# Optimization experiments

Measured on AMD Instinct MI355X. Metric: run time of the kernel, lower is better.

## Reference

```python
import jax, jax.numpy as jnp
import numpy as np

CONF = 0.3      # confidence threshold (NMS.conf)
IOU = 0.6       # IoU threshold (NMS.iou)
MAX_WH = 4096.0 # class-offset trick for per-class NMS
K = 2048        # max candidates entering NMS (yolov5-style cap)
MAX_DET = 300   # max detections kept per image (fixed output size)


def setup_inputs() -> dict:
    key = jax.random.key(0)
    kxy, kwh, kobj, kcls = jax.random.split(key, 4)
    B, N, NC = 8, 25200, 80
    # realistic raw predictions: xywh in pixel units for a 640x640 image
    xy = jax.random.uniform(kxy, (B, N, 2), minval=0.0, maxval=640.0)
    wh = jax.random.uniform(kwh, (B, N, 2), minval=2.0, maxval=160.0)
    obj = jax.random.uniform(kobj, (B, N, 1))
    cls = jax.random.uniform(kcls, (B, N, NC))
    x = jnp.concatenate([xy, wh, obj, cls], axis=-1)  # [B, N, 5+NC]
    return {"x": x}


def _xywh2xyxy(b):
    xy, half = b[..., :2], b[..., 2:4] * 0.5
    return jnp.concatenate([xy - half, xy + half], axis=-1)


def _pairwise_iou(boxes):  # boxes: [K, 4] xyxy -> [K, K]
    lt = jnp.maximum(boxes[:, None, :2], boxes[None, :, :2])
    rb = jnp.minimum(boxes[:, None, 2:], boxes[None, :, 2:])
    inter = jnp.clip(rb - lt, 0.0).prod(-1)
    area = (boxes[:, 2] - boxes[:, 0]) * (boxes[:, 3] - boxes[:, 1])
    return inter / (area[:, None] + area[None, :] - inter + 1e-9)


def _nms_single(pred):  # pred: [N, 5+NC]
    obj = pred[:, 4]
    cls_conf = pred[:, 5:] * obj[:, None]          # conf = obj * cls prob
    conf = cls_conf.max(-1)
    cls_id = jnp.argmax(cls_conf, -1)
    valid = (obj > CONF) & (conf > CONF)           # candidate + final threshold
    boxes = _xywh2xyxy(pred[:, :4])
    scores = jnp.where(valid, conf, -1.0)
    top_s, idx = jax.lax.top_k(scores, K)          # cap candidates, sorted desc
    boxes_k = boxes[idx]
    cls_k = cls_id[idx]
    valid_k = top_s > 0.0
    # offset boxes by class so NMS is per-class
    shifted = boxes_k + cls_k[:, None].astype(boxes_k.dtype) * MAX_WH
    iou = _pairwise_iou(shifted)                   # [K, K]
    order = jnp.arange(K)

    def body(keep, i):  # greedy suppression in score order
        active = keep[i] & valid_k[i]
        sup = (iou[i] > IOU) & (order > i)
        keep = jnp.where(active, keep & ~sup, keep)
        return keep, None

    keep, _ = jax.lax.scan(body, jnp.ones((K,), bool), order)
    keep = keep & valid_k
    final_s = jnp.where(keep, top_s, -1.0)
    det_s, det_i = jax.lax.top_k(final_s, MAX_DET)
    dets = jnp.concatenate(
        [boxes_k[det_i], top_s[det_i][:, None],
         cls_k[det_i][:, None].astype(boxes_k.dtype)], axis=-1)  # [MAX_DET, 6]
    return dets, det_s > 0.0


def reference(x):
    # returns (dets [B, MAX_DET, 6] = xyxy,conf,cls ; valid mask [B, MAX_DET])
    return jax.vmap(_nms_single)(x)
```

## Files before the change

kernel.cpp:

```cpp
#include <hip/hip_runtime.h>

#define B 8
#define N 25200
#define ROW 85
#define NC 80
#define K 2048
#define MAXDET 300
#define NBUCKET 16384
#define CAND_CAP 4096
#define NCHUNK 32
#define STILE 64
#define CTR_STRIDE 64

__global__ void __launch_bounds__(256)
nms_score_kernel(const float* __restrict__ x,
                 float* __restrict__ scores,
                 int* __restrict__ cls_id,
                 float4* __restrict__ boxes4,
                 unsigned* __restrict__ ready,
                 unsigned* __restrict__ done_ctr) {
    int b = blockIdx.y;
    int i0 = blockIdx.x * STILE;
    if (blockIdx.x == 0 && threadIdx.x == 0) {
        ready[b * CTR_STRIDE] = 0u;
        done_ctr[b * CTR_STRIDE] = 0u;
    }
    int rows = N - i0; if (rows > STILE) rows = STILE;
    __shared__ float lx[STILE * ROW];
    {
        const float4* s4 = (const float4*)(x + ((size_t)b * N + i0) * ROW);
        float4* d4 = (float4*)lx;
        int nv = rows * ROW / 4;
        for (int k = threadIdx.x; k < nv; k += 256) d4[k] = s4[k];
    }
    __syncthreads();
    int g = threadIdx.x >> 2;
    int q = threadIdx.x & 3;
    if (g >= rows) return;
    const float* p = lx + g * ROW;
    float obj = p[4];
    float best = -1e30f;
    int bc = 127;
    if (obj > 0.3f) {
        #pragma unroll
        for (int k = 0; k < 20; ++k) {
            int c = q + 4 * k;
            float v = __fmul_rn(p[5 + c], obj);
            if (v > best) { best = v; bc = c; }
        }
    }
    #pragma unroll
    for (int m = 1; m < 4; m <<= 1) {
        float ov = __shfl_xor(best, m, 64);
        int   oc = __shfl_xor(bc, m, 64);
        if (ov > best || (ov == best && oc < bc)) { best = ov; bc = oc; }
    }
    if (q == 0) {
        int i = i0 + g;
        float score = (obj > 0.3f && best > 0.3f) ? best : -1.0f;
        scores[b * N + i] = score;
        cls_id[b * N + i] = (bc == 127) ? 0 : bc;
        float cx = p[0], cy = p[1], w = p[2], h = p[3];
        float hx = __fmul_rn(w, 0.5f);
        float hy = __fmul_rn(h, 0.5f);
        boxes4[b * N + i] = make_float4(__fsub_rn(cx, hx), __fsub_rn(cy, hy),
                                        __fadd_rn(cx, hx), __fadd_rn(cy, hy));
    }
}

__global__ void __launch_bounds__(1024, 1)
nms_tail_kernel(const float* __restrict__ scores,
                const float4* __restrict__ boxes4,
                const int* __restrict__ cls_id,
                unsigned long long* __restrict__ gkeys,
                unsigned long long* __restrict__ keepbits,
                unsigned* __restrict__ ready,
                unsigned* __restrict__ done_ctr,
                float* __restrict__ out) {
    __shared__ union {
        struct {
            unsigned loff[NBUCKET];
            unsigned lcnt16[NBUCKET / 2];
            unsigned long long lk[CAND_CAP];
        } s;
        struct {
            unsigned long long keys[K];
            unsigned long long lcm[NC * NCHUNK];
        } c;
    } U;
    __shared__ unsigned wsum[16];

    int bid = blockIdx.x;
    int t = threadIdx.x;
    int ln = t & 63, wv = t >> 6;
    unsigned long long below = (ln == 0) ? 0ULL : (~0ULL >> (64 - ln));

    if (bid < B) {
        int b = bid;
        constexpr int NITER = (N + 1023) / 1024;

        if (t < NCHUNK) keepbits[b * NCHUNK + t] = 0ULL;
        {
            uint4 z = {0u, 0u, 0u, 0u};
            uint4* d1 = (uint4*)U.s.loff;
            for (int k = t; k < (NBUCKET + NBUCKET / 2) / 4; k += 1024) d1[k] = z;
        }
        for (int k = t; k < CAND_CAP; k += 1024) U.s.lk[k] = 0ULL;
        __syncthreads();

        float sreg[NITER];
        #pragma unroll
        for (int r = 0; r < NITER; ++r) {
            int i = t + r * 1024;
            float s = (i < N) ? scores[b * N + i] : -1.0f;
            sreg[r] = s;
            if (s > 0.0f) {
                int q = (int)(__fmul_rn(s, 16384.0f));
                if (q > NBUCKET - 1) q = NBUCKET - 1;
                atomicAdd(&U.s.loff[q], 1u);
            }
        }
        __syncthreads();

        unsigned v[16];
        unsigned A4 = (unsigned)(NBUCKET - 16 - t * 16) / 4;
        {
            uint4 u0 = ((uint4*)U.s.loff)[A4 + 0];
            uint4 u1 = ((uint4*)U.s.loff)[A4 + 1];
            uint4 u2 = ((uint4*)U.s.loff)[A4 + 2];
            uint4 u3 = ((uint4*)U.s.loff)[A4 + 3];
            unsigned u[16] = {u0.x,u0.y,u0.z,u0.w, u1.x,u1.y,u1.z,u1.w,
                              u2.x,u2.y,u2.z,u2.w, u3.x,u3.y,u3.z,u3.w};
            #pragma unroll
            for (int k = 0; k < 16; ++k) v[k] = u[15 - k];
        }
        unsigned S = 0;
        #pragma unroll
        for (int k = 0; k < 16; ++k) S += v[k];
        unsigned pref = S;
        #pragma unroll
        for (int o = 1; o < 64; o <<= 1) { unsigned u = __shfl_up(pref, o, 64); if (ln >= o) pref += u; }
        if (ln == 63) wsum[wv] = pref;
        __syncthreads();
        unsigned wbase = 0;
        for (int w = 0; w < wv; ++w) wbase += wsum[w];
        unsigned running = wbase + pref - S;
        {
            unsigned o[16];
            #pragma unroll
            for (int k = 0; k < 16; ++k) { o[15 - k] = running; running += v[k]; }
            ((uint4*)U.s.loff)[A4 + 0] = make_uint4(o[0],  o[1],  o[2],  o[3]);
            ((uint4*)U.s.loff)[A4 + 1] = make_uint4(o[4],  o[5],  o[6],  o[7]);
            ((uint4*)U.s.loff)[A4 + 2] = make_uint4(o[8],  o[9],  o[10], o[11]);
            ((uint4*)U.s.loff)[A4 + 3] = make_uint4(o[12], o[13], o[14], o[15]);
        }
        __syncthreads();

        #pragma unroll
        for (int r = 0; r < NITER; ++r) {
            float s = sreg[r];
            if (s > 0.0f) {
                int i = t + r * 1024;
                int q = (int)(__fmul_rn(s, 16384.0f));
                if (q > NBUCKET - 1) q = NBUCKET - 1;
                unsigned start = U.s.loff[q];
                if (start < CAND_CAP) {
                    unsigned sh = (q & 1) * 16;
                    unsigned old = atomicAdd(&U.s.lcnt16[q >> 1], 1u << sh);
                    unsigned rank = (old >> sh) & 0xFFFFu;
                    unsigned pos = start + rank;
                    if (pos < CAND_CAP) {
                        unsigned long long key =
                            ((unsigned long long)__float_as_uint(s) << 32) | (unsigned)(~i);
                        U.s.lk[pos] = key;
                    }
                }
            }
        }
        __syncthreads();

        for (int q = t; q < NBUCKET; q += 1024) {
            unsigned start = U.s.loff[q];
            if (start < CAND_CAP) {
                unsigned c = (U.s.lcnt16[q >> 1] >> ((q & 1) * 16)) & 0xFFFFu;
                unsigned m = c;
                if (m > CAND_CAP - start) m = CAND_CAP - start;
                if (m >= 2) {
                    for (unsigned a = start + 1; a < start + m; ++a) {
                        unsigned long long kv = U.s.lk[a];
                        unsigned p2 = a;
                        while (p2 > start && U.s.lk[p2 - 1] < kv) { U.s.lk[p2] = U.s.lk[p2 - 1]; --p2; }
                        U.s.lk[p2] = kv;
                    }
                }
            }
        }
        __syncthreads();

        for (int r = t; r < K; r += 1024)
            gkeys[(size_t)b * K + r] = U.s.lk[r];
        __syncthreads();
        if (t == 0) {
            __threadfence();
            atomicExch(&ready[b * CTR_STRIDE], 1u);
        }
        return;
    }

    int gid = bid - B;
    int b = gid / 5;
    int grp = gid % 5;
    int c = grp * 16 + wv;

    if (t == 0) {
        while (atomicOr(&ready[b * CTR_STRIDE], 0u) == 0u)
            __builtin_amdgcn_s_sleep(8);
        __threadfence();
    }
    __syncthreads();

    for (int r = t; r < K; r += 1024) U.c.keys[r] = gkeys[(size_t)b * K + r];
    for (int k = t; k < NC * NCHUNK; k += 1024) U.c.lcm[k] = 0ULL;
    __syncthreads();

    for (int r = t; r < K; r += 1024) {
        unsigned long long key = U.c.keys[r];
        if (key != 0ULL) {
            int idx = (int)(~(unsigned)key);
            int cc = cls_id[b * N + idx];
            atomicOr(&U.c.lcm[cc * NCHUNK + (r >> 6)], 1ULL << (r & 63));
        }
    }
    __syncthreads();

    int n = 0, r = -1, ch_i = -1, myk = -1;
    unsigned long long mych = 0ULL;
    for (int ch = 0; ch < NCHUNK; ++ch) {
        unsigned long long m = U.c.lcm[c * NCHUNK + ch];
        int cnt = __popcll(m);
        if (myk < 0 && ln < n + cnt) { mych = m; myk = ln - n; ch_i = ch; }
        n += cnt;
    }
    if (myk >= 0) {
        unsigned long long mm = mych;
        for (int z = 0; z < myk; ++z) mm &= mm - 1;
        r = ch_i * 64 + (int)__builtin_ctzll(mm);
    }

    float shf = __fmul_rn((float)c, 4096.0f);

    if (n > 0 && n <= 64) {
        float x1 = 0.f, y1 = 0.f, x2 = 0.f, y2 = 0.f, ar = 0.f;
        if (ln < n) {
            unsigned long long key = U.c.keys[r];
            int idx = (int)(~(unsigned)key);
            float4 bb = boxes4[(size_t)b * N + idx];
            x1 = __fadd_rn(bb.x, shf); y1 = __fadd_rn(bb.y, shf);
            x2 = __fadd_rn(bb.z, shf); y2 = __fadd_rn(bb.w, shf);
            ar = __fmul_rn(__fsub_rn(x2, x1), __fsub_rn(y2, y1));
        }
        unsigned long long keepw = (n == 64) ? ~0ULL : ((1ULL << n) - 1ULL);
        for (int i = 0; i < n; ++i) {
            if (!((keepw >> i) & 1ULL)) continue;
            float bx1 = __shfl(x1, i, 64), by1 = __shfl(y1, i, 64);
            float bx2 = __shfl(x2, i, 64), by2 = __shfl(y2, i, 64);
            float ba  = __shfl(ar, i, 64);
            bool cond = false;
            if (ln > i && ln < n) {
                float lx = fmaxf(bx1, x1), ly = fmaxf(by1, y1);
                float rx = fminf(bx2, x2), ry = fminf(by2, y2);
                float w = fmaxf(__fsub_rn(rx, lx), 0.0f);
                float h = fmaxf(__fsub_rn(ry, ly), 0.0f);
                float inter = __fmul_rn(w, h);
                float denom = __fadd_rn(__fsub_rn(__fadd_rn(ba, ar), inter), 1e-9f);
                cond = __fdiv_rn(inter, denom) > 0.6f;
            }
            keepw &= ~__ballot(cond);
        }
        if (ln < n && ((keepw >> ln) & 1ULL))
            atomicOr(&keepbits[b * NCHUNK + (r >> 6)], 1ULL << (r & 63));
    } else if (n > 64) {
        unsigned long long membw = (ln < NCHUNK) ? U.c.lcm[c * NCHUNK + ln] : 0ULL;
        unsigned long long keepw2 = membw;
        for (int i = 0; i < K; ++i) {
            int ch = i >> 6;
            unsigned long long mw = __shfl(membw, ch, 64);
            unsigned long long kw = __shfl(keepw2, ch, 64);
            unsigned long long bi = 1ULL << (i & 63);
            if (!(mw & kw & bi)) continue;
            unsigned long long keyi = U.c.keys[i];
            int idxi = (int)(~(unsigned)keyi);
            float4 bi4 = boxes4[(size_t)b * N + idxi];
            float bx1 = __fadd_rn(bi4.x, shf), by1 = __fadd_rn(bi4.y, shf);
            float bx2 = __fadd_rn(bi4.z, shf), by2 = __fadd_rn(bi4.w, shf);
            float ba = __fmul_rn(__fsub_rn(bx2, bx1), __fsub_rn(by2, by1));
            for (int c2 = ch; c2 < NCHUNK; ++c2) {
                int j = c2 * 64 + ln;
                unsigned long long mw2 = __shfl(membw, c2, 64);
                bool cond = false;
                if (j > i && ((mw2 >> ln) & 1ULL)) {
                    unsigned long long keyj = U.c.keys[j];
                    int idxj = (int)(~(unsigned)keyj);
                    float4 bj4 = boxes4[(size_t)b * N + idxj];
                    float x1 = __fadd_rn(bj4.x, shf), y1 = __fadd_rn(bj4.y, shf);
                    float x2 = __fadd_rn(bj4.z, shf), y2 = __fadd_rn(bj4.w, shf);
                    float arj = __fmul_rn(__fsub_rn(x2, x1), __fsub_rn(y2, y1));
                    float lx = fmaxf(bx1, x1), ly = fmaxf(by1, y1);
                    float rx = fminf(bx2, x2), ry = fminf(by2, y2);
                    float w = fmaxf(__fsub_rn(rx, lx), 0.0f);
                    float h = fmaxf(__fsub_rn(ry, ly), 0.0f);
                    float inter = __fmul_rn(w, h);
                    float denom = __fadd_rn(__fsub_rn(__fadd_rn(ba, arj), inter), 1e-9f);
                    cond = __fdiv_rn(inter, denom) > 0.6f;
                }
                unsigned long long sup = __ballot(cond);
                if (ln == c2) keepw2 &= ~sup;
            }
        }
        if (ln < NCHUNK && (keepw2 & membw))
            atomicOr(&keepbits[b * NCHUNK + ln], keepw2 & membw);
    }

    __threadfence();
    unsigned old = 0;
    if (ln == 0) old = atomicAdd(&done_ctr[b * CTR_STRIDE], 1u);
    old = (unsigned)__shfl((int)old, 0, 64);
    if (old == NC - 1) {
        __threadfence();
        unsigned long long kw = 0ULL;
        if (ln < NCHUNK) kw = atomicOr(&keepbits[b * NCHUNK + ln], 0ULL);
        int total = 0;
        for (int ch = 0; ch < NCHUNK; ++ch) total += __popcll(__shfl(kw, ch, 64));

        float* dets  = out + (size_t)b * MAXDET * 6;
        float* flags = out + (size_t)B * MAXDET * 6 + (size_t)b * MAXDET;
        int kc = 0, nc2 = 0;
        for (int ch = 0; ch < NCHUNK; ++ch) {
            int i = ch * 64 + ln;
            unsigned long long m = __shfl(kw, ch, 64);
            bool k = ((m >> ln) & 1ULL) != 0ULL;
            int pc = __popcll(m);
            int slot = k ? (kc + __popcll(m & below))
                         : (total + nc2 + __popcll((~m) & below));
            if (slot < MAXDET) {
                unsigned long long key = U.c.keys[i];
                float s, ox1, oy1, ox2, oy2; int oc;
                if (key == 0ULL) {
                    s = -1.0f; ox1 = oy1 = ox2 = oy2 = 0.0f; oc = 0;
                } else {
                    s = __uint_as_float((unsigned)(key >> 32));
                    int idx = (int)(~(unsigned)key);
                    float4 bb = boxes4[(size_t)b * N + idx];
                    ox1 = bb.x; oy1 = bb.y; ox2 = bb.z; oy2 = bb.w;
                    oc = cls_id[b * N + idx];
                }
                dets[slot * 6 + 0] = ox1;
                dets[slot * 6 + 1] = oy1;
                dets[slot * 6 + 2] = ox2;
                dets[slot * 6 + 3] = oy2;
                dets[slot * 6 + 4] = s;
                dets[slot * 6 + 5] = (float)oc;
                flags[slot] = k ? 1.0f : 0.0f;
            }
            kc += pc;
            nc2 += 64 - pc;
        }
    }
}

extern "C" void kernel_launch(void* const* d_in, const int* in_sizes, int n_in,
                              void* d_out, int out_size, void* d_ws, size_t ws_size,
                              hipStream_t stream) {
    const float* x = (const float*)d_in[0];
    float* out = (float*)d_out;

    char* ws = (char*)d_ws;
    size_t off = 0;
    auto alloc = [&](size_t bytes) -> void* {
        void* p = ws + off;
        off += bytes;
        off = (off + 255) & ~(size_t)255;
        return p;
    };

    float*    scores = (float*)    alloc((size_t)B * N * 4);
    int*      cls_id = (int*)      alloc((size_t)B * N * 4);
    float4*   boxes4 = (float4*)   alloc((size_t)B * N * 16);
    unsigned long long* gkeys    = (unsigned long long*) alloc((size_t)B * K * 8);
    unsigned long long* keepbits = (unsigned long long*) alloc((size_t)B * NCHUNK * 8);
    unsigned* ready    = (unsigned*) alloc((size_t)B * CTR_STRIDE * 4);
    unsigned* done_ctr = (unsigned*) alloc((size_t)B * CTR_STRIDE * 4);
    (void)ws_size;

    nms_score_kernel<<<dim3((N + STILE - 1) / STILE, B), 256, 0, stream>>>(
        x, scores, cls_id, boxes4, ready, done_ctr);
    nms_tail_kernel<<<B + 5 * B, 1024, 0, stream>>>(
        scores, boxes4, cls_id, gkeys, keepbits, ready, done_ctr, out);
}
```

Baseline: 141.3 us.

## Shrink histogram buckets and parallelize final output write across whole block

Cuts the score histogram from 16384 to 4096 buckets, which shrinks the shared-memory zeroing and the prefix scan to one uint4 per thread. It moves the keepbits zeroing into the score kernel, and it changes the final output stage. Previously a single wavefront walked all 32 chunks serially; now the last block computes per-chunk prefix counts in shared memory and all 16 wavefronts write two chunks each. Coarser buckets may put more ties into one bucket, which risks bucket overflow near the candidate cap.

```diff
diff --git a/kernel.cpp b/kernel.cpp
--- a/kernel.cpp
+++ b/kernel.cpp
@@ -6,7 +6,7 @@
 #define NC 80
 #define K 2048
 #define MAXDET 300
-#define NBUCKET 16384
+#define NBUCKET 4096
 #define CAND_CAP 4096
 #define NCHUNK 32
 #define STILE 64
@@ -18,12 +18,16 @@
                  int* __restrict__ cls_id,
                  float4* __restrict__ boxes4,
                  unsigned* __restrict__ ready,
-                 unsigned* __restrict__ done_ctr) {
+                 unsigned* __restrict__ done_ctr,
+                 unsigned long long* __restrict__ keepbits) {
     int b = blockIdx.y;
     int i0 = blockIdx.x * STILE;
-    if (blockIdx.x == 0 && threadIdx.x == 0) {
-        ready[b * CTR_STRIDE] = 0u;
-        done_ctr[b * CTR_STRIDE] = 0u;
+    if (blockIdx.x == 0) {
+        if (threadIdx.x == 0) {
+            ready[b * CTR_STRIDE] = 0u;
+            done_ctr[b * CTR_STRIDE] = 0u;
+        }
+        if (threadIdx.x < NCHUNK) keepbits[b * NCHUNK + threadIdx.x] = 0ULL;
     }
     int rows = N - i0; if (rows > STILE) rows = STILE;
     __shared__ float lx[STILE * ROW];
@@ -86,6 +90,10 @@
         struct {
             unsigned long long keys[K];
             unsigned long long lcm[NC * NCHUNK];
+            unsigned long long kept[NCHUNK];
+            unsigned kcpref[NCHUNK];
+            int total;
+            int oflag;
         } c;
     } U;
     __shared__ unsigned wsum[16];
@@ -99,7 +107,6 @@
         int b = bid;
         constexpr int NITER = (N + 1023) / 1024;
 
-        if (t < NCHUNK) keepbits[b * NCHUNK + t] = 0ULL;
         {
             uint4 z = {0u, 0u, 0u, 0u};
             uint4* d1 = (uint4*)U.s.loff;
@@ -115,28 +122,20 @@
             float s = (i < N) ? scores[b * N + i] : -1.0f;
             sreg[r] = s;
             if (s > 0.0f) {
-                int q = (int)(__fmul_rn(s, 16384.0f));
+                int q = (int)(__fmul_rn(s, 4096.0f));
                 if (q > NBUCKET - 1) q = NBUCKET - 1;
                 atomicAdd(&U.s.loff[q], 1u);
             }
         }
         __syncthreads();
 
-        unsigned v[16];
-        unsigned A4 = (unsigned)(NBUCKET - 16 - t * 16) / 4;
+        unsigned v[4];
+        unsigned A4 = (unsigned)(NBUCKET / 4 - 1 - t);
         {
-            uint4 u0 = ((uint4*)U.s.loff)[A4 + 0];
-            uint4 u1 = ((uint4*)U.s.loff)[A4 + 1];
-            uint4 u2 = ((uint4*)U.s.loff)[A4 + 2];
-            uint4 u3 = ((uint4*)U.s.loff)[A4 + 3];
-            unsigned u[16] = {u0.x,u0.y,u0.z,u0.w, u1.x,u1.y,u1.z,u1.w,
-                              u2.x,u2.y,u2.z,u2.w, u3.x,u3.y,u3.z,u3.w};
-            #pragma unroll
-            for (int k = 0; k < 16; ++k) v[k] = u[15 - k];
-        }
-        unsigned S = 0;
-        #pragma unroll
-        for (int k = 0; k < 16; ++k) S += v[k];
+            uint4 u0 = ((uint4*)U.s.loff)[A4];
+            v[0] = u0.w; v[1] = u0.z; v[2] = u0.y; v[3] = u0.x;
+        }
+        unsigned S = v[0] + v[1] + v[2] + v[3];
         unsigned pref = S;
         #pragma unroll
         for (int o = 1; o < 64; o <<= 1) { unsigned u = __shfl_up(pref, o, 64); if (ln >= o) pref += u; }
@@ -146,13 +145,10 @@
         for (int w = 0; w < wv; ++w) wbase += wsum[w];
         unsigned running = wbase + pref - S;
         {
-            unsigned o[16];
+            unsigned o[4];
             #pragma unroll
-            for (int k = 0; k < 16; ++k) { o[15 - k] = running; running += v[k]; }
-            ((uint4*)U.s.loff)[A4 + 0] = make_uint4(o[0],  o[1],  o[2],  o[3]);
-            ((uint4*)U.s.loff)[A4 + 1] = make_uint4(o[4],  o[5],  o[6],  o[7]);
-            ((uint4*)U.s.loff)[A4 + 2] = make_uint4(o[8],  o[9],  o[10], o[11]);
-            ((uint4*)U.s.loff)[A4 + 3] = make_uint4(o[12], o[13], o[14], o[15]);
+            for (int k = 0; k < 4; ++k) { o[3 - k] = running; running += v[k]; }
+            ((uint4*)U.s.loff)[A4] = make_uint4(o[0], o[1], o[2], o[3]);
         }
         __syncthreads();
 
@@ -161,7 +157,7 @@
             float s = sreg[r];
             if (s > 0.0f) {
                 int i = t + r * 1024;
-                int q = (int)(__fmul_rn(s, 16384.0f));
+                int q = (int)(__fmul_rn(s, 4096.0f));
                 if (q > NBUCKET - 1) q = NBUCKET - 1;
                 unsigned start = U.s.loff[q];
                 if (start < CAND_CAP) {
@@ -213,6 +209,7 @@
     int c = grp * 16 + wv;
 
     if (t == 0) {
+        U.c.oflag = 0;
         while (atomicOr(&ready[b * CTR_STRIDE], 0u) == 0u)
             __builtin_amdgcn_s_sleep(8);
         __threadfence();
@@ -327,21 +324,35 @@
     old = (unsigned)__shfl((int)old, 0, 64);
     if (old == NC - 1) {
         __threadfence();
-        unsigned long long kw = 0ULL;
-        if (ln < NCHUNK) kw = atomicOr(&keepbits[b * NCHUNK + ln], 0ULL);
-        int total = 0;
-        for (int ch = 0; ch < NCHUNK; ++ch) total += __popcll(__shfl(kw, ch, 64));
-
+        unsigned long long kwv = 0ULL;
+        if (ln < NCHUNK) kwv = atomicOr(&keepbits[b * NCHUNK + ln], 0ULL);
+        unsigned pc = (unsigned)__popcll(kwv);
+        unsigned incl = pc;
+        #pragma unroll
+        for (int o = 1; o < 32; o <<= 1) { unsigned u = __shfl_up(incl, o, 64); if (ln >= o) incl += u; }
+        if (ln < NCHUNK) {
+            U.c.kept[ln] = kwv;
+            U.c.kcpref[ln] = incl - pc;
+        }
+        if (ln == 31) U.c.total = (int)incl;
+        if (ln == 0)  U.c.oflag = 1;
+    }
+    __syncthreads();
+
+    if (U.c.oflag) {
+        int total = U.c.total;
         float* dets  = out + (size_t)b * MAXDET * 6;
         float* flags = out + (size_t)B * MAXDET * 6 + (size_t)b * MAXDET;
-        int kc = 0, nc2 = 0;
-        for (int ch = 0; ch < NCHUNK; ++ch) {
+        #pragma unroll
+        for (int h = 0; h < 2; ++h) {
+            int ch = wv * 2 + h;
             int i = ch * 64 + ln;
-            unsigned long long m = __shfl(kw, ch, 64);
+            unsigned long long m = U.c.kept[ch];
             bool k = ((m >> ln) & 1ULL) != 0ULL;
-            int pc = __popcll(m);
-            int slot = k ? (kc + __popcll(m & below))
-                         : (total + nc2 + __popcll((~m) & below));
+            int kp = (int)U.c.kcpref[ch];
+            int np = ch * 64 - kp;
+            int slot = k ? (kp + (int)__popcll(m & below))
+                         : (total + np + (int)__popcll((~m) & below));
             if (slot < MAXDET) {
                 unsigned long long key = U.c.keys[i];
                 float s, ox1, oy1, ox2, oy2; int oc;
@@ -362,8 +373,6 @@
                 dets[slot * 6 + 5] = (float)oc;
                 flags[slot] = k ? 1.0f : 0.0f;
             }
-            kc += pc;
-            nc2 += 64 - pc;
         }
     }
 }
@@ -393,7 +402,7 @@
     (void)ws_size;
 
     nms_score_kernel<<<dim3((N + STILE - 1) / STILE, B), 256, 0, stream>>>(
-        x, scores, cls_id, boxes4, ready, done_ctr);
+        x, scores, cls_id, boxes4, ready, done_ctr, keepbits);
     nms_tail_kernel<<<B + 5 * B, 1024, 0, stream>>>(
         scores, boxes4, cls_id, gkeys, keepbits, ready, done_ctr, out);
 }
```

Result: no change. 139.6 us (-1.2%).
